# Kernel optimization log

Hardware: AMD Instinct MI355X
Metric: run time of the kernel (lower is better)

## Reference

```python
import jax, jax.numpy as jnp
import numpy as np

B, LQ, LK, D, H = 8, 1024, 1024, 1024, 8
DH = D // H  # per-head dim (att_units // num_heads, and V head dim since V = k)
LN_EPS = 1e-5


def setup_inputs() -> dict:
    key = jax.random.key(0)
    ks = jax.random.split(key, 8)
    s = 1.0 / np.sqrt(D)
    return {
        "q": jax.random.normal(ks[0], (B, LQ, D), dtype=jnp.float32),
        "k": jax.random.normal(ks[1], (B, LK, D), dtype=jnp.float32),
        "Wq": jax.random.normal(ks[2], (D, D), dtype=jnp.float32) * s,
        "bq": jnp.zeros((D,), dtype=jnp.float32),
        "Wk": jax.random.normal(ks[3], (D, D), dtype=jnp.float32) * s,
        "bk": jnp.zeros((D,), dtype=jnp.float32),
        "ln_gamma": jnp.ones((D,), dtype=jnp.float32),
        "ln_beta": jnp.zeros((D,), dtype=jnp.float32),
    }


def _layer_norm(x, gamma, beta):
    mu = jnp.mean(x, axis=-1, keepdims=True)
    var = jnp.mean(jnp.square(x - mu), axis=-1, keepdims=True)
    return (x - mu) * jax.lax.rsqrt(var + LN_EPS) * gamma + beta


def reference(q, k, Wq, bq, Wk, bk, ln_gamma, ln_beta):
    # q: [B, LQ, D], k: [B, LK, D]
    Q = q @ Wq + bq                      # [B, LQ, D]
    K = k @ Wk + bk                      # [B, LK, D]
    V = k                                # V is the raw key input (no projection)
    Qh = Q.reshape(B, LQ, H, DH)         # split(att_units//H, -1)+concat(0) == head reshape
    Kh = K.reshape(B, LK, H, DH)
    Vh = V.reshape(B, LK, H, DH)
    sim = jnp.einsum("bqhd,bkhd->bhqk", Qh, Kh) / np.sqrt(DH).astype(np.float32)
    attn = jax.nn.softmax(sim, axis=-1)  # [B, H, LQ, LK]
    att_h = jnp.einsum("bhqk,bkhd->bqhd", attn, Vh).reshape(B, LQ, D)
    att_h = att_h * 0.1 + q * 0.9        # residual blend
    att_h = _layer_norm(att_h, ln_gamma, ln_beta)
    return att_h  # ff_units_list == [] -> ff is None -> ff_h = att_h
```

## Files before the change

### kernel.cpp

```cpp
#include <hip/hip_runtime.h>
#include <hip/hip_bf16.h>
#include <cstdint>

#define BATCH 8
#define SEQ   1024
#define DMODEL 1024
#define NHEAD 8
#define DHEAD 128

using short8 = __attribute__((ext_vector_type(8))) short;
using f32x4  = __attribute__((ext_vector_type(4))) float;
typedef unsigned short u16;

__device__ inline u16 f2bf(float f) {
    union { float f; uint32_t u; } v; v.f = f;
    uint32_t r = (v.u + 0x7FFFu + ((v.u >> 16) & 1u)) >> 16;
    return (u16)r;
}

__device__ inline float exp2_fast(float x) { return __builtin_amdgcn_exp2f(x); }

__device__ inline uint32_t cvtpk_bf16(float a, float b) {
    uint32_t r;
    asm("v_cvt_pk_bf16_f32 %0, %1, %2" : "=v"(r) : "v"(a), "v"(b));
    return r;
}

#define GLL16(g, l)                                                                        \
    __builtin_amdgcn_global_load_lds((__attribute__((address_space(1))) const uint32_t*)(g), \
                                     (__attribute__((address_space(3))) uint32_t*)(l), 16, 0, 0)

__global__ void transpose_conv(const float* __restrict__ Wq,
                               const float* __restrict__ Wk,
                               const float* __restrict__ kin,
                               const float* __restrict__ qin,
                               u16* __restrict__ WqT,
                               u16* __restrict__ WkT,
                               u16* __restrict__ Vt,
                               u16* __restrict__ kb,
                               u16* __restrict__ qb) {
    __shared__ float tile[32][33];
    int z = blockIdx.z;
    const float* src;
    u16* dst;
    u16* sdst = nullptr;
    const float* qsrc = nullptr;
    u16* qdst = nullptr;
    if (z == 0)      { src = Wq; dst = WqT; }
    else if (z == 1) { src = Wk; dst = WkT; }
    else {
        size_t off = (size_t)(z - 2) * DMODEL * SEQ;
        src  = kin + off;
        dst  = Vt  + off;
        sdst = kb  + off;
        qsrc = qin + off;
        qdst = qb  + off;
    }
    int x  = blockIdx.x * 32 + threadIdx.x;
    int y0 = blockIdx.y * 32;
    for (int i = threadIdx.y; i < 32; i += 8) {
        float v = src[(size_t)(y0 + i) * 1024 + x];
        tile[i][threadIdx.x] = v;
        if (sdst) sdst[(size_t)(y0 + i) * 1024 + x] = f2bf(v);
    }
    if (qsrc) {
        for (int i = threadIdx.y; i < 32; i += 8)
            qdst[(size_t)(y0 + i) * 1024 + x] = f2bf(qsrc[(size_t)(y0 + i) * 1024 + x]);
    }
    __syncthreads();
    int xo  = y0 + threadIdx.x;
    int yo0 = blockIdx.x * 32;
    for (int i = threadIdx.y; i < 32; i += 8)
        dst[(size_t)(yo0 + i) * 1024 + xo] = f2bf(tile[threadIdx.x][i]);
}

__global__ __launch_bounds__(256, 4) void gemm_dual(const u16* __restrict__ Aq,
                                                    const u16* __restrict__ Ak,
                                                    const u16* __restrict__ BTq,
                                                    const u16* __restrict__ BTk,
                                                    const float* __restrict__ biasq,
                                                    const float* __restrict__ biask,
                                                    u16* __restrict__ Outq,
                                                    u16* __restrict__ Outk) {
    __shared__ __align__(16) u16 As[2][128 * 32];
    __shared__ __align__(16) u16 Bs[2][128 * 32];

    int bid = blockIdx.x;
    int half = bid >> 9;
    int b2 = bid & 511;
    const u16* A  = half ? Ak  : Aq;
    const u16* BT = half ? BTk : BTq;
    const float* bias = half ? biask : biasq;
    u16* Out = half ? Outk : Outq;
    float scale = half ? 1.0f : (0.08838834764831845f * 1.4426950408889634f);

    int swz = (b2 & 7) * 64 + (b2 >> 3);
    int mt = swz >> 3, nt = swz & 7;
    int m0 = mt * 128, n0 = nt * 128;

    int t = threadIdx.x, lane = t & 63, w = t >> 6;
    int wm = w >> 1, wn = w & 1;
    int lr = lane & 15, lg = lane >> 4;

    const u16* pa[2];
    const u16* pb[2];
#pragma unroll
    for (int i = 0; i < 2; ++i) {
        int L = (w * 2 + i) * 64 + lane;
        int rp = L >> 3, ss = L & 7;
        int u = ss ^ (rp & 7);
        int row = (rp << 1) | (u >> 2);
        int g = u & 3;
        pa[i] = A  + (size_t)(m0 + row) * 1024 + g * 8;
        pb[i] = BT + (size_t)(n0 + row) * 1024 + g * 8;
    }
    int aoff[4], boff[4];
#pragma unroll
    for (int f = 0; f < 4; ++f) {
        int rowA = wm * 64 + f * 16 + lr;
        int sA = (((rowA & 1) << 2) | lg) ^ ((rowA >> 1) & 7);
        aoff[f] = (rowA >> 1) * 64 + sA * 8;
        int rowB = wn * 64 + f * 16 + lr;
        int sB = (((rowB & 1) << 2) | lg) ^ ((rowB >> 1) & 7);
        boff[f] = (rowB >> 1) * 64 + sB * 8;
    }

    f32x4 acc[4][4] = {};

#define GSTAGE(buf)                                         \
    {                                                       \
        _Pragma("unroll")                                   \
        for (int i = 0; i < 2; ++i) {                       \
            GLL16(pa[i], &As[buf][(w * 2 + i) * 512]);      \
            GLL16(pb[i], &Bs[buf][(w * 2 + i) * 512]);      \
            pa[i] += 32;                                    \
            pb[i] += 32;                                    \
        }                                                   \
    }

    GSTAGE(0);
    __syncthreads();

    int cur = 0;
    for (int k0 = 0; k0 < DMODEL; k0 += 32) {
        if (k0 + 32 < DMODEL) GSTAGE(cur ^ 1);
        short8 af[4], bfr[4];
#pragma unroll
        for (int f = 0; f < 4; ++f) {
            af[f]  = *(const short8*)&As[cur][aoff[f]];
            bfr[f] = *(const short8*)&Bs[cur][boff[f]];
        }
        __builtin_amdgcn_s_setprio(1);
#pragma unroll
        for (int fm = 0; fm < 4; ++fm)
#pragma unroll
            for (int fn = 0; fn < 4; ++fn)
                acc[fm][fn] = __builtin_amdgcn_mfma_f32_16x16x32_bf16(af[fm], bfr[fn], acc[fm][fn], 0, 0, 0);
        __builtin_amdgcn_s_setprio(0);
        __syncthreads();
        cur ^= 1;
    }
#undef GSTAGE

#pragma unroll
    for (int fn = 0; fn < 4; ++fn) {
        int col = n0 + wn * 64 + fn * 16 + lr;
        float bv = bias[col];
#pragma unroll
        for (int fm = 0; fm < 4; ++fm)
#pragma unroll
            for (int j = 0; j < 4; ++j) {
                int row = m0 + wm * 64 + fm * 16 + lg * 4 + j;
                Out[(size_t)row * 1024 + col] = f2bf((acc[fm][fn][j] + bv) * scale);
            }
    }
}

__global__ __launch_bounds__(512, 2) void attn_kernel(const u16* __restrict__ Qb,
                                                      const u16* __restrict__ Kb,
                                                      const u16* __restrict__ Vt,
                                                      float* __restrict__ AO,
                                                      u16* __restrict__ AOb) {
    __shared__ __align__(16) u16 Kbuf[2][64 * 128];
    __shared__ __align__(16) u16 Vbuf[2][128 * 64];
    __shared__ __align__(16) u16 Pl[8][2][16 * 64];

    int bid = blockIdx.x;
    int swz = (bid & 7) * 32 + (bid >> 3);
    int bh  = swz >> 2;
    int qt  = swz & 3;
    int b = bh >> 3, h = bh & 7;
    int q0 = qt * 256;

    int t = threadIdx.x, lane = t & 63, w = t >> 6;
    int lr = lane & 15, lg = lane >> 4;

    short8 qfA[4], qfB[4];
    {
        size_t qa = (size_t)(b * SEQ + q0 + w * 32 + lr) * 1024 + h * DHEAD;
        size_t qbB = qa + (size_t)16 * 1024;
#pragma unroll
        for (int kk = 0; kk < 4; ++kk) {
            qfA[kk] = *(const short8*)&Qb[qa  + kk * 32 + lg * 8];
            qfB[kk] = *(const short8*)&Qb[qbB + kk * 32 + lg * 8];
        }
    }

    float mA = -1e30f, lA = 0.f, mB = -1e30f, lB = 0.f;
    f32x4 oA[8] = {}, oB[8] = {};
    u16* PwA = &Pl[w][0][0];
    u16* PwB = &Pl[w][1][0];
    const int pwrow = lr * 64;
    const int lx = lr & 7;

#define STAGE(nb, kk0)                                                                   \
    {                                                                                    \
        _Pragma("unroll")                                                                \
        for (int i = 0; i < 2; ++i) {                                                    \
            int g = (w * 2 + i) * 64 + lane;                                             \
            int row = g >> 4, cp = g & 15;                                               \
            int c = cp ^ (row & 7);                                                      \
            const u16* src = Kb + ((size_t)(b * SEQ + (kk0) + row) * 1024 + h * 128 + c * 8); \
            GLL16(src, &Kbuf[nb][(w * 2 + i) * 512]);                                    \
        }                                                                                \
        _Pragma("unroll")                                                                \
        for (int i = 0; i < 2; ++i) {                                                    \
            int g = (w * 2 + i) * 64 + lane;                                             \
            int d = g >> 3, cp = g & 7;                                                  \
            int c = cp ^ (d & 7);                                                        \
            const u16* src = Vt + ((size_t)(bh * 128 + d) * 1024 + (kk0) + c * 8);       \
            GLL16(src, &Vbuf[nb][(w * 2 + i) * 512]);                                    \
        }                                                                                \
    }

    STAGE(0, 0);
    __syncthreads();

    int cur = 0;
    for (int k0 = 0; k0 < SEQ; k0 += 64) {
        if (k0 + 64 < SEQ) STAGE(cur ^ 1, k0 + 64);

        const u16* Kc = &Kbuf[cur][0];
        f32x4 sA[4] = {}, sB[4] = {};
        __builtin_amdgcn_s_setprio(1);
#pragma unroll
        for (int fn = 0; fn < 4; ++fn) {
            int krow = (fn * 16 + lr) * 128;
#pragma unroll
            for (int kk = 0; kk < 4; ++kk) {
                short8 kf = *(const short8*)&Kc[krow + (((kk * 4 + lg) ^ lx) << 3)];
                sA[fn] = __builtin_amdgcn_mfma_f32_16x16x32_bf16(kf, qfA[kk], sA[fn], 0, 0, 0);
                sB[fn] = __builtin_amdgcn_mfma_f32_16x16x32_bf16(kf, qfB[kk], sB[fn], 0, 0, 0);
            }
        }
        __builtin_amdgcn_s_setprio(0);

        {
            float pm0 = fmaxf(fmaxf(sA[0][0], sA[0][1]), fmaxf(sA[0][2], sA[0][3]));
            float pm1 = fmaxf(fmaxf(sA[1][0], sA[1][1]), fmaxf(sA[1][2], sA[1][3]));
            float pm2 = fmaxf(fmaxf(sA[2][0], sA[2][1]), fmaxf(sA[2][2], sA[2][3]));
            float pm3 = fmaxf(fmaxf(sA[3][0], sA[3][1]), fmaxf(sA[3][2], sA[3][3]));
            float pmax = fmaxf(fmaxf(pm0, pm1), fmaxf(pm2, pm3));
            if (__any(pmax > mA + 11.5416f)) {
                float rm = pmax;
                rm = fmaxf(rm, __shfl_xor(rm, 16));
                rm = fmaxf(rm, __shfl_xor(rm, 32));
                float mnew = fmaxf(mA, rm);
                float alpha = exp2_fast(mA - mnew);
                mA = mnew;
                lA *= alpha;
#pragma unroll
                for (int db = 0; db < 8; ++db) oA[db] *= alpha;
            }
            float p[4][4];
            float ls0 = 0.f, ls1 = 0.f, ls2 = 0.f, ls3 = 0.f;
#pragma unroll
            for (int j = 0; j < 4; ++j) {
                p[0][j] = exp2_fast(sA[0][j] - mA); ls0 += p[0][j];
                p[1][j] = exp2_fast(sA[1][j] - mA); ls1 += p[1][j];
                p[2][j] = exp2_fast(sA[2][j] - mA); ls2 += p[2][j];
                p[3][j] = exp2_fast(sA[3][j] - mA); ls3 += p[3][j];
            }
            lA += (ls0 + ls1) + (ls2 + ls3);
#pragma unroll
            for (int fn = 0; fn < 4; ++fn) {
                uint2 pk;
                pk.x = cvtpk_bf16(p[fn][0], p[fn][1]);
                pk.y = cvtpk_bf16(p[fn][2], p[fn][3]);
                int idx = pwrow + (((fn * 2 + (lg >> 1)) ^ lx) << 3) + ((lg & 1) << 2);
                *(uint2*)&PwA[idx] = pk;
            }
        }
        {
            float pm0 = fmaxf(fmaxf(sB[0][0], sB[0][1]), fmaxf(sB[0][2], sB[0][3]));
            float pm1 = fmaxf(fmaxf(sB[1][0], sB[1][1]), fmaxf(sB[1][2], sB[1][3]));
            float pm2 = fmaxf(fmaxf(sB[2][0], sB[2][1]), fmaxf(sB[2][2], sB[2][3]));
            float pm3 = fmaxf(fmaxf(sB[3][0], sB[3][1]), fmaxf(sB[3][2], sB[3][3]));
            float pmax = fmaxf(fmaxf(pm0, pm1), fmaxf(pm2, pm3));
            if (__any(pmax > mB + 11.5416f)) {
                float rm = pmax;
                rm = fmaxf(rm, __shfl_xor(rm, 16));
                rm = fmaxf(rm, __shfl_xor(rm, 32));
                float mnew = fmaxf(mB, rm);
                float alpha = exp2_fast(mB - mnew);
                mB = mnew;
                lB *= alpha;
#pragma unroll
                for (int db = 0; db < 8; ++db) oB[db] *= alpha;
            }
            float p[4][4];
            float ls0 = 0.f, ls1 = 0.f, ls2 = 0.f, ls3 = 0.f;
#pragma unroll
            for (int j = 0; j < 4; ++j) {
                p[0][j] = exp2_fast(sB[0][j] - mB); ls0 += p[0][j];
                p[1][j] = exp2_fast(sB[1][j] - mB); ls1 += p[1][j];
                p[2][j] = exp2_fast(sB[2][j] - mB); ls2 += p[2][j];
                p[3][j] = exp2_fast(sB[3][j] - mB); ls3 += p[3][j];
            }
            lB += (ls0 + ls1) + (ls2 + ls3);
#pragma unroll
            for (int fn = 0; fn < 4; ++fn) {
                uint2 pk;
                pk.x = cvtpk_bf16(p[fn][0], p[fn][1]);
                pk.y = cvtpk_bf16(p[fn][2], p[fn][3]);
                int idx = pwrow + (((fn * 2 + (lg >> 1)) ^ lx) << 3) + ((lg & 1) << 2);
                *(uint2*)&PwB[idx] = pk;
            }
        }

        const u16* Vc = &Vbuf[cur][0];
        short8 pfA0 = *(const short8*)&PwA[pwrow + ((lg ^ lx) << 3)];
        short8 pfA1 = *(const short8*)&PwA[pwrow + (((4 + lg) ^ lx) << 3)];
        short8 pfB0 = *(const short8*)&PwB[pwrow + ((lg ^ lx) << 3)];
        short8 pfB1 = *(const short8*)&PwB[pwrow + (((4 + lg) ^ lx) << 3)];
        __builtin_amdgcn_s_setprio(1);
#pragma unroll
        for (int db = 0; db < 8; ++db) {
            int vr = (db * 16 + lr) * 64;
            short8 v0 = *(const short8*)&Vc[vr + ((lg ^ lx) << 3)];
            short8 v1 = *(const short8*)&Vc[vr + (((4 + lg) ^ lx) << 3)];
            oA[db] = __builtin_amdgcn_mfma_f32_16x16x32_bf16(v0, pfA0, oA[db], 0, 0, 0);
            oA[db] = __builtin_amdgcn_mfma_f32_16x16x32_bf16(v1, pfA1, oA[db], 0, 0, 0);
            oB[db] = __builtin_amdgcn_mfma_f32_16x16x32_bf16(v0, pfB0, oB[db], 0, 0, 0);
            oB[db] = __builtin_amdgcn_mfma_f32_16x16x32_bf16(v1, pfB1, oB[db], 0, 0, 0);
        }
        __builtin_amdgcn_s_setprio(0);

        __syncthreads();
        cur ^= 1;
    }

    float ltA = lA;
    ltA += __shfl_xor(ltA, 16);
    ltA += __shfl_xor(ltA, 32);
    float invA = 1.f / ltA;
    float ltB = lB;
    ltB += __shfl_xor(ltB, 16);
    ltB += __shfl_xor(ltB, 32);
    float invB = 1.f / ltB;
    size_t obaseA = (size_t)(b * SEQ + q0 + w * 32 + lr) * 1024 + h * DHEAD + lg * 4;
    size_t obaseB = obaseA + (size_t)16 * 1024;
    if (AOb) {
#pragma unroll
        for (int db = 0; db < 8; ++db) {
            uint2 pa, pb2;
            pa.x = cvtpk_bf16(oA[db][0] * invA, oA[db][1] * invA);
            pa.y = cvtpk_bf16(oA[db][2] * invA, oA[db][3] * invA);
            pb2.x = cvtpk_bf16(oB[db][0] * invB, oB[db][1] * invB);
            pb2.y = cvtpk_bf16(oB[db][2] * invB, oB[db][3] * invB);
            *(uint2*)&AOb[obaseA + db * 16] = pa;
            *(uint2*)&AOb[obaseB + db * 16] = pb2;
        }
    } else {
#pragma unroll
        for (int db = 0; db < 8; ++db) {
            float4 ov;
            ov.x = oA[db][0] * invA;
            ov.y = oA[db][1] * invA;
            ov.z = oA[db][2] * invA;
            ov.w = oA[db][3] * invA;
            *(float4*)&AO[obaseA + db * 16] = ov;
            float4 ow;
            ow.x = oB[db][0] * invB;
            ow.y = oB[db][1] * invB;
            ow.z = oB[db][2] * invB;
            ow.w = oB[db][3] * invB;
            *(float4*)&AO[obaseB + db * 16] = ow;
        }
    }
#undef STAGE
}

__global__ __launch_bounds__(256) void ln_kernel(const float* __restrict__ AOf,
                                                 const u16* __restrict__ AOb,
                                                 const float* __restrict__ qin,
                                                 const float* __restrict__ gamma,
                                                 const float* __restrict__ beta,
                                                 float* __restrict__ out) {
    __shared__ float red[8];
    int row = blockIdx.x;
    int t = threadIdx.x;
    size_t base = (size_t)row * 1024 + t * 4;

    float a0, a1, a2, a3;
    if (AOb) {
        ushort4 u = *(const ushort4*)&AOb[base];
        union { uint32_t i; float f; } c0, c1, c2, c3;
        c0.i = (uint32_t)u.x << 16; c1.i = (uint32_t)u.y << 16;
        c2.i = (uint32_t)u.z << 16; c3.i = (uint32_t)u.w << 16;
        a0 = c0.f; a1 = c1.f; a2 = c2.f; a3 = c3.f;
    } else {
        float4 a = *(const float4*)&AOf[base];
        a0 = a.x; a1 = a.y; a2 = a.z; a3 = a.w;
    }
    float4 qq = *(const float4*)&qin[base];
    float x0 = a0 * 0.1f + qq.x * 0.9f;
    float x1 = a1 * 0.1f + qq.y * 0.9f;
    float x2 = a2 * 0.1f + qq.z * 0.9f;
    float x3 = a3 * 0.1f + qq.w * 0.9f;

    float s  = x0 + x1 + x2 + x3;
    float s2 = x0 * x0 + x1 * x1 + x2 * x2 + x3 * x3;
    for (int d = 1; d < 64; d <<= 1) {
        s  += __shfl_xor(s, d);
        s2 += __shfl_xor(s2, d);
    }
    int w = t >> 6, lane = t & 63;
    if (lane == 0) { red[w] = s; red[4 + w] = s2; }
    __syncthreads();
    s  = red[0] + red[1] + red[2] + red[3];
    s2 = red[4] + red[5] + red[6] + red[7];

    float mu   = s * (1.f / 1024.f);
    float var  = s2 * (1.f / 1024.f) - mu * mu;
    float rstd = rsqrtf(var + 1e-5f);

    float4 g  = *(const float4*)&gamma[t * 4];
    float4 be = *(const float4*)&beta[t * 4];
    float4 o;
    o.x = (x0 - mu) * rstd * g.x + be.x;
    o.y = (x1 - mu) * rstd * g.y + be.y;
    o.z = (x2 - mu) * rstd * g.z + be.z;
    o.w = (x3 - mu) * rstd * g.w + be.w;
    *(float4*)&out[base] = o;
}

extern "C" void kernel_launch(void* const* d_in, const int* in_sizes, int n_in,
                              void* d_out, int out_size, void* d_ws, size_t ws_size,
                              hipStream_t stream) {
    const float* q     = (const float*)d_in[0];
    const float* k     = (const float*)d_in[1];
    const float* Wq    = (const float*)d_in[2];
    const float* bq    = (const float*)d_in[3];
    const float* Wk    = (const float*)d_in[4];
    const float* bk    = (const float*)d_in[5];
    const float* gamma = (const float*)d_in[6];
    const float* beta  = (const float*)d_in[7];
    float* out = (float*)d_out;

    char* ws = (char*)d_ws;
    u16* WqT = (u16*)ws;
    u16* WkT = (u16*)(ws + (size_t)(2  << 20));
    u16* Qb  = (u16*)(ws + (size_t)(4  << 20));
    u16* Kb  = (u16*)(ws + (size_t)(20 << 20));
    u16* Vt  = (u16*)(ws + (size_t)(36 << 20));
    u16* AOb = (ws_size >= ((size_t)68 << 20)) ? (u16*)(ws + ((size_t)52 << 20)) : nullptr;

    u16* qb = (u16*)d_out;
    u16* kb = qb + (size_t)8 * 1024 * 1024;

    transpose_conv<<<dim3(32, 32, 2 + BATCH), dim3(32, 8), 0, stream>>>(Wq, Wk, k, q, WqT, WkT, Vt, kb, qb);

    gemm_dual<<<1024, 256, 0, stream>>>(qb, kb, WqT, WkT, bq, bk, Qb, Kb);

    attn_kernel<<<256, 512, 0, stream>>>(Qb, Kb, Vt, out, AOb);

    ln_kernel<<<8192, 256, 0, stream>>>(out, AOb, q, gamma, beta, out);
}
```

Baseline: 128.4 us.

## Software-pipeline PV matmul one tile behind QK in attention loop

The attention loop now runs the P·V MFMAs for the previous key tile right after the current tile's Q·K^T MFMAs, before the softmax of the current tile. K/V shared buffers become triple-buffered so the previous V tile stays resident, and the P fragments are carried in registers across iterations. A final epilogue applies the last tile's P·V after the loop. The aim is to interleave matrix-core work with the exp/max softmax math. The cost is more LDS and extra live VGPRs, which could hurt occupancy or cause spills.

```diff
diff --git a/kernel.cpp b/kernel.cpp
--- a/kernel.cpp
+++ b/kernel.cpp
@@ -181,8 +181,8 @@
                                                       const u16* __restrict__ Vt,
                                                       float* __restrict__ AO,
                                                       u16* __restrict__ AOb) {
-    __shared__ __align__(16) u16 Kbuf[2][64 * 128];
-    __shared__ __align__(16) u16 Vbuf[2][128 * 64];
+    __shared__ __align__(16) u16 Kbuf[3][64 * 128];
+    __shared__ __align__(16) u16 Vbuf[3][128 * 64];
     __shared__ __align__(16) u16 Pl[8][2][16 * 64];
 
     int bid = blockIdx.x;
@@ -208,6 +208,7 @@
 
     float mA = -1e30f, lA = 0.f, mB = -1e30f, lB = 0.f;
     f32x4 oA[8] = {}, oB[8] = {};
+    short8 pfA0p = {}, pfA1p = {}, pfB0p = {}, pfB1p = {};
     u16* PwA = &Pl[w][0][0];
     u16* PwB = &Pl[w][1][0];
     const int pwrow = lr * 64;
@@ -236,9 +237,9 @@
     STAGE(0, 0);
     __syncthreads();
 
-    int cur = 0;
+    int cur = 0, nxt = 1, prv = 2;
     for (int k0 = 0; k0 < SEQ; k0 += 64) {
-        if (k0 + 64 < SEQ) STAGE(cur ^ 1, k0 + 64);
+        if (k0 + 64 < SEQ) STAGE(nxt, k0 + 64);
 
         const u16* Kc = &Kbuf[cur][0];
         f32x4 sA[4] = {}, sB[4] = {};
@@ -254,6 +255,20 @@
             }
         }
         __builtin_amdgcn_s_setprio(0);
+
+        if (k0 > 0) {
+            const u16* Vc = &Vbuf[prv][0];
+#pragma unroll
+            for (int db = 0; db < 8; ++db) {
+                int vr = (db * 16 + lr) * 64;
+                short8 v0 = *(const short8*)&Vc[vr + ((lg ^ lx) << 3)];
+                short8 v1 = *(const short8*)&Vc[vr + (((4 + lg) ^ lx) << 3)];
+                oA[db] = __builtin_amdgcn_mfma_f32_16x16x32_bf16(v0, pfA0p, oA[db], 0, 0, 0);
+                oA[db] = __builtin_amdgcn_mfma_f32_16x16x32_bf16(v1, pfA1p, oA[db], 0, 0, 0);
+                oB[db] = __builtin_amdgcn_mfma_f32_16x16x32_bf16(v0, pfB0p, oB[db], 0, 0, 0);
+                oB[db] = __builtin_amdgcn_mfma_f32_16x16x32_bf16(v1, pfB1p, oB[db], 0, 0, 0);
+            }
+        }
 
         {
             float pm0 = fmaxf(fmaxf(sA[0][0], sA[0][1]), fmaxf(sA[0][2], sA[0][3]));
@@ -328,26 +343,29 @@
             }
         }
 
-        const u16* Vc = &Vbuf[cur][0];
-        short8 pfA0 = *(const short8*)&PwA[pwrow + ((lg ^ lx) << 3)];
-        short8 pfA1 = *(const short8*)&PwA[pwrow + (((4 + lg) ^ lx) << 3)];
-        short8 pfB0 = *(const short8*)&PwB[pwrow + ((lg ^ lx) << 3)];
-        short8 pfB1 = *(const short8*)&PwB[pwrow + (((4 + lg) ^ lx) << 3)];
+        pfA0p = *(const short8*)&PwA[pwrow + ((lg ^ lx) << 3)];
+        pfA1p = *(const short8*)&PwA[pwrow + (((4 + lg) ^ lx) << 3)];
+        pfB0p = *(const short8*)&PwB[pwrow + ((lg ^ lx) << 3)];
+        pfB1p = *(const short8*)&PwB[pwrow + (((4 + lg) ^ lx) << 3)];
+
+        __syncthreads();
+        int tmp = prv; prv = cur; cur = nxt; nxt = tmp;
+    }
+
+    {
+        const u16* Vc = &Vbuf[prv][0];
         __builtin_amdgcn_s_setprio(1);
 #pragma unroll
         for (int db = 0; db < 8; ++db) {
             int vr = (db * 16 + lr) * 64;
             short8 v0 = *(const short8*)&Vc[vr + ((lg ^ lx) << 3)];
             short8 v1 = *(const short8*)&Vc[vr + (((4 + lg) ^ lx) << 3)];
-            oA[db] = __builtin_amdgcn_mfma_f32_16x16x32_bf16(v0, pfA0, oA[db], 0, 0, 0);
-            oA[db] = __builtin_amdgcn_mfma_f32_16x16x32_bf16(v1, pfA1, oA[db], 0, 0, 0);
-            oB[db] = __builtin_amdgcn_mfma_f32_16x16x32_bf16(v0, pfB0, oB[db], 0, 0, 0);
-            oB[db] = __builtin_amdgcn_mfma_f32_16x16x32_bf16(v1, pfB1, oB[db], 0, 0, 0);
+            oA[db] = __builtin_amdgcn_mfma_f32_16x16x32_bf16(v0, pfA0p, oA[db], 0, 0, 0);
+            oA[db] = __builtin_amdgcn_mfma_f32_16x16x32_bf16(v1, pfA1p, oA[db], 0, 0, 0);
+            oB[db] = __builtin_amdgcn_mfma_f32_16x16x32_bf16(v0, pfB0p, oB[db], 0, 0, 0);
+            oB[db] = __builtin_amdgcn_mfma_f32_16x16x32_bf16(v1, pfB1p, oB[db], 0, 0, 0);
         }
         __builtin_amdgcn_s_setprio(0);
-
-        __syncthreads();
-        cur ^= 1;
     }
 
     float ltA = lA;
```

Measured after the change: 130.7 us. About the same (+1.8%).
